# Kernel optimization log

Measured on AMD Instinct MI355X. Metric: run time of the kernel, lower is better.

The kernel has to match this reference:

```python
import jax, jax.numpy as jnp
import numpy as np

B, C, W, H = 256, 1, 512, 512
D0, D1 = 64, 64            # input_dims: crop/resample target
LATENT = 1024
HIST = 8                   # transformer_history_size (also attention heads)
DEPTH = 4
HEADS = 8
DIM_HEAD = 64              # n_heads arg is used as dim_head
INNER = HEADS * DIM_HEAD   # 512
MLP = LATENT
NCLS = 1000
EPS = 1e-5
RESNET_GAIN = 2.0 ** 7     # 7 identity ResidualBlocks, each does x += x


def setup_inputs() -> dict:
    key = jax.random.key(0)
    ks = jax.random.split(key, 12)
    def rn(k, shape):
        return jax.random.normal(k, shape, jnp.float32) * 0.02
    return dict(
        x=jax.random.normal(ks[0], (B, C, W, H), jnp.float32),
        transformation=jax.random.uniform(ks[1], (B, 4), dtype=jnp.float32),
        history=jnp.zeros((HIST, B, LATENT), jnp.float32),
        w_img=rn(ks[2], (D0 * D1, LATENT)), b_img=jnp.zeros((LATENT,), jnp.float32),
        ln1_s=jnp.ones((DEPTH, LATENT), jnp.float32), ln1_b=jnp.zeros((DEPTH, LATENT), jnp.float32),
        w_qkv=rn(ks[3], (DEPTH, LATENT, 3 * INNER)),
        w_o=rn(ks[4], (DEPTH, INNER, LATENT)), b_o=jnp.zeros((DEPTH, LATENT), jnp.float32),
        ln2_s=jnp.ones((DEPTH, LATENT), jnp.float32), ln2_b=jnp.zeros((DEPTH, LATENT), jnp.float32),
        w_ff1=rn(ks[5], (DEPTH, LATENT, MLP)), b_ff1=jnp.zeros((DEPTH, MLP), jnp.float32),
        w_ff2=rn(ks[6], (DEPTH, MLP, LATENT)), b_ff2=jnp.zeros((DEPTH, LATENT), jnp.float32),
        w_cls=rn(ks[7], (HIST * LATENT, NCLS)), b_cls=jnp.zeros((NCLS,), jnp.float32),
        w_tr=rn(ks[8], (HIST * LATENT, 4)), b_tr=jnp.zeros((4,), jnp.float32),
    )


def _ln(x, s, b):
    m = x.mean(-1, keepdims=True)
    v = x.var(-1, keepdims=True)
    return (x - m) / jnp.sqrt(v + EPS) * s + b


def _crop_one(img, sc):
    # img [C,W,H], sc = [px, py, zx, zy]; nearest crop+resample to (D0, D1)
    px, py, zx, zy = sc[0], sc[1], sc[2], sc[3]
    x1 = px * (W - D0)
    y1 = py * (H - D1)
    xs = jnp.minimum(W - x1, zx * (W - D0) + D0)
    ys = jnp.minimum(H - y1, zy * (H - D1) + D1)
    xi = jnp.clip((jnp.floor(jnp.arange(D0, dtype=jnp.float32) / D0 * xs) + x1).astype(jnp.int32), 0, W - 1)
    yi = jnp.clip((jnp.floor(jnp.arange(D1, dtype=jnp.float32) / D1 * ys) + y1).astype(jnp.int32), 0, H - 1)
    # itertools.product(c, xi, yi) ordering == reshape(-1) of [C, D0, D1]
    return img[:, xi[:, None], yi[None, :]].reshape(-1)


def _forward(x, transformation, history, w_img, b_img, ln1_s, ln1_b, w_qkv, w_o, b_o,
             ln2_s, ln2_b, w_ff1, b_ff1, w_ff2, b_ff2, w_cls, b_cls, w_tr, b_tr):
    crops = jax.vmap(_crop_one)(x, transformation)          # [B, C*D0*D1]
    feats = crops * RESNET_GAIN                             # ResNet18 == scale by 2^7
    image_latent = feats @ w_img + b_img                    # [B, LATENT]
    # history.append(latent); take last HIST; stack dim=1 -> [B, HIST, LATENT]
    hist = jnp.transpose(history, (1, 0, 2))                # [B, HIST, LATENT]
    z = jnp.concatenate([hist[:, 1:], image_latent[:, None, :]], axis=1)
    scale = DIM_HEAD ** -0.5
    for i in range(DEPTH):
        h = _ln(z, ln1_s[i], ln1_b[i])
        qkv = h @ w_qkv[i]                                  # [B, HIST, 3*INNER]
        q, k, v = jnp.split(qkv, 3, axis=-1)
        q = q.reshape(B, HIST, HEADS, DIM_HEAD).transpose(0, 2, 1, 3)
        k = k.reshape(B, HIST, HEADS, DIM_HEAD).transpose(0, 2, 1, 3)
        v = v.reshape(B, HIST, HEADS, DIM_HEAD).transpose(0, 2, 1, 3)
        attn = jax.nn.softmax(jnp.einsum('bhid,bhjd->bhij', q, k) * scale, axis=-1)
        o = jnp.einsum('bhij,bhjd->bhid', attn, v).transpose(0, 2, 1, 3).reshape(B, HIST, INNER)
        z = o @ w_o[i] + b_o[i] + z
        h2 = _ln(z, ln2_s[i], ln2_b[i])
        z = jax.nn.gelu(h2 @ w_ff1[i] + b_ff1[i], approximate=False) @ w_ff2[i] + b_ff2[i] + z
    tl = z.reshape(B, HIST * LATENT)
    class_pred = tl @ w_cls + b_cls                         # [B, NCLS]
    transform_pred = jax.nn.sigmoid(tl @ w_tr + b_tr)       # [B, 4]
    return class_pred, transform_pred


def reference(x, transformation, history, w_img, b_img, ln1_s, ln1_b, w_qkv, w_o, b_o,
              ln2_s, ln2_b, w_ff1, b_ff1, w_ff2, b_ff2, w_cls, b_cls, w_tr, b_tr):
    return _forward(x, transformation, history, w_img, b_img, ln1_s, ln1_b, w_qkv, w_o, b_o,
                    ln2_s, ln2_b, w_ff1, b_ff1, w_ff2, b_ff2, w_cls, b_cls, w_tr, b_tr)
```

## Files before the change

kernel.cpp:

```cpp
#include <hip/hip_runtime.h>
#include <cstdint>
#include <cstddef>

typedef __attribute__((ext_vector_type(8))) __bf16 bf16x8;
typedef __attribute__((ext_vector_type(8))) unsigned short u16x8;
typedef __attribute__((ext_vector_type(4))) float f32x4;
typedef __attribute__((ext_vector_type(4))) unsigned short u16x4;

__device__ __forceinline__ unsigned short f2bf(float f) {
  unsigned int u = __builtin_bit_cast(unsigned int, f);
  u += 0x7fffu + ((u >> 16) & 1u);
  return (unsigned short)(u >> 16);
}
__device__ __forceinline__ float bf2f(unsigned short u) {
  return __builtin_bit_cast(float, ((unsigned int)u) << 16);
}

__device__ void wcast_tile(char* smemc, int bid,
    const float* s_img, const float* s_qkv, const float* s_o,
    const float* s_ff1, const float* s_ff2, const float* s_cls,
    unsigned short* d_img, unsigned short* d_qkv, unsigned short* d_o,
    unsigned short* d_ff1, unsigned short* d_ff2, unsigned short* d_cls) {
  float (*tile)[65] = (float (*)[65])smemc;
  const float* src; unsigned short* dst; int K, N, Npad, rel;
  if (bid < 1024)       { src = s_img; dst = d_img; K = 4096; N = 1024; Npad = 1024; rel = bid; }
  else if (bid < 2560)  { rel = bid - 1024; int l = rel / 384; rel -= l * 384;
                          src = s_qkv + (size_t)l * 1024 * 1536; dst = d_qkv + (size_t)l * 1536 * 1024;
                          K = 1024; N = 1536; Npad = 1536; }
  else if (bid < 3072)  { rel = bid - 2560; int l = rel / 128; rel -= l * 128;
                          src = s_o   + (size_t)l * 512 * 1024;  dst = d_o   + (size_t)l * 1024 * 512;
                          K = 512;  N = 1024; Npad = 1024; }
  else if (bid < 4096)  { rel = bid - 3072; int l = rel / 256; rel -= l * 256;
                          src = s_ff1 + (size_t)l * 1024 * 1024; dst = d_ff1 + (size_t)l * 1024 * 1024;
                          K = 1024; N = 1024; Npad = 1024; }
  else if (bid < 5120)  { rel = bid - 4096; int l = rel / 256; rel -= l * 256;
                          src = s_ff2 + (size_t)l * 1024 * 1024; dst = d_ff2 + (size_t)l * 1024 * 1024;
                          K = 1024; N = 1024; Npad = 1024; }
  else                  { rel = bid - 5120; src = s_cls; dst = d_cls; K = 8192; N = 1000; Npad = 1024; }
  int tilesX = Npad >> 6;
  int nx = rel % tilesX, ky = rel / tilesX;
  int n0 = nx << 6, k0 = ky << 6;
  int t = threadIdx.x;
#pragma unroll
  for (int i = 0; i < 4; ++i) {
    int slot = t + i * 256;
    int kk = slot >> 4, cq = slot & 15;
    int n = n0 + cq * 4;
    float4 v;
    if (n + 3 < N) v = *(const float4*)(src + (size_t)(k0 + kk) * N + n);
    else {
      v.x = v.y = v.z = v.w = 0.0f;
      if (n < N)     v.x = src[(size_t)(k0 + kk) * N + n];
      if (n + 1 < N) v.y = src[(size_t)(k0 + kk) * N + n + 1];
      if (n + 2 < N) v.z = src[(size_t)(k0 + kk) * N + n + 2];
      if (n + 3 < N) v.w = src[(size_t)(k0 + kk) * N + n + 3];
    }
    tile[kk][cq * 4 + 0] = v.x;
    tile[kk][cq * 4 + 1] = v.y;
    tile[kk][cq * 4 + 2] = v.z;
    tile[kk][cq * 4 + 3] = v.w;
  }
  __syncthreads();
#pragma unroll
  for (int i = 0; i < 4; ++i) {
    int slot = t + i * 256;
    int n = slot >> 4, kq = slot & 15;
    u16x4 o;
    o.x = f2bf(tile[kq * 4 + 0][n]);
    o.y = f2bf(tile[kq * 4 + 1][n]);
    o.z = f2bf(tile[kq * 4 + 2][n]);
    o.w = f2bf(tile[kq * 4 + 3][n]);
    *(u16x4*)(dst + (size_t)(n0 + n) * K + k0 + kq * 4) = o;
  }
}

template <int BK, int ITERS>
__device__ __forceinline__ void stage_tile(const unsigned short* __restrict__ g, int ld,
                                           int k0, char* lbase, int tid) {
  constexpr int CH = BK / 8;
#pragma unroll
  for (int it = 0; it < ITERS; ++it) {
    int c = tid + it * 256;
    int r = c / CH;
    int slot = c & (CH - 1);
    int gc = slot ^ (r & (CH - 1));
    const unsigned short* src = g + (size_t)r * ld + (k0 + gc * 8);
    char* dst = lbase + c * 16;
    __builtin_amdgcn_global_load_lds((__attribute__((address_space(1))) void*)src,
                                     (__attribute__((address_space(3))) void*)dst, 16, 0, 0);
  }
}

template <int BK>
__device__ __forceinline__ bf16x8 ld_frag(const char* base, int row, int k8) {
  constexpr int CH = BK / 8;
  int off = row * (BK * 2) + ((k8 ^ (row & (CH - 1))) << 4);
  return *(const bf16x8*)(base + off);
}

template <int TN, int ACT, int OMODE, bool RES, int BK>
__device__ void gemm_tile(char* smem,
    const unsigned short* __restrict__ A, int lda,
    const unsigned short* __restrict__ BT, int ldb, int Kloop,
    const float* __restrict__ bias, const float* __restrict__ res,
    float* __restrict__ outF, unsigned short* __restrict__ outB,
    int ldC, int Nstore, int m0, int n0, int koff) {
  constexpr int MR = (TN == 64) ? 2 : 4;
  constexpr int ABYTES = 128 * BK * 2;
  constexpr int BUFS = (128 + TN) * BK * 2;
  constexpr int AITERS = BK / 16;
  constexpr int BITERS = TN * BK / 2048;
  const int tid = threadIdx.x;
  const int lane = tid & 63;
  const int wid = tid >> 6;
  const int rowbase = (TN == 64) ? wid * 32 : (wid >> 1) * 64;
  const int colbase = (TN == 64) ? 0 : (wid & 1) * 64;
  const unsigned short* Ag = A + (size_t)m0 * lda + koff;
  const unsigned short* Bg = BT + (size_t)n0 * ldb + koff;
  f32x4 acc[MR][4];
#pragma unroll
  for (int m = 0; m < MR; m++)
#pragma unroll
    for (int n = 0; n < 4; n++) acc[m][n] = 0.f;
  const int nt = Kloop / BK;
  stage_tile<BK, AITERS>(Ag, lda, 0, smem, tid);
  stage_tile<BK, BITERS>(Bg, ldb, 0, smem + ABYTES, tid);
  __syncthreads();
  int cur = 0;
  const int rA = lane & 15, kq = lane >> 4;
  for (int t = 0; t < nt; ++t) {
    if (t + 1 < nt) {
      stage_tile<BK, AITERS>(Ag, lda, (t + 1) * BK, smem + (cur ^ 1) * BUFS, tid);
      stage_tile<BK, BITERS>(Bg, ldb, (t + 1) * BK, smem + (cur ^ 1) * BUFS + ABYTES, tid);
    }
    const char* la = smem + cur * BUFS;
    const char* lb = la + ABYTES;
#pragma unroll
    for (int kk = 0; kk < BK / 32; ++kk) {
      int k8 = kk * 4 + kq;
      bf16x8 af[MR], bfr[4];
#pragma unroll
      for (int m = 0; m < MR; m++) af[m] = ld_frag<BK>(la, rowbase + m * 16 + rA, k8);
#pragma unroll
      for (int n = 0; n < 4; n++) bfr[n] = ld_frag<BK>(lb, colbase + n * 16 + rA, k8);
#pragma unroll
      for (int m = 0; m < MR; m++)
#pragma unroll
        for (int n = 0; n < 4; n++)
          acc[m][n] = __builtin_amdgcn_mfma_f32_16x16x32_bf16(af[m], bfr[n], acc[m][n], 0, 0, 0);
    }
    __syncthreads();
    cur ^= 1;
  }
  const int rb = m0 + rowbase + (kq << 2);
  const int cb = n0 + colbase + rA;
#pragma unroll
  for (int m = 0; m < MR; m++)
#pragma unroll
    for (int n = 0; n < 4; n++) {
      int cg = cb + n * 16;
      if (cg >= Nstore) continue;
      float bv = bias ? bias[cg] : 0.0f;
#pragma unroll
      for (int j = 0; j < 4; j++) {
        int rg = rb + m * 16 + j;
        float v = acc[m][n][j] + bv;
        if (RES) v += res[(size_t)rg * ldC + cg];
        if (ACT == 1) v = 0.5f * v * (1.0f + erff(v * 0.70710678118654752f));
        if (OMODE == 0) {
          outF[(size_t)rg * ldC + cg] = v;
        } else if (OMODE == 1) {
          outB[(size_t)rg * ldC + cg] = f2bf(v);
        } else {
          outF[(size_t)rg * ldC + cg] = v;
          outB[(size_t)rg * ldC + cg] = f2bf(v);
        }
      }
    }
}

#define SLABW 200
__global__ __launch_bounds__(256) void qkvattn(
    const unsigned short* __restrict__ h,
    const unsigned short* __restrict__ BTq,
    unsigned short* __restrict__ obuf) {
  __shared__ __align__(16) char smem[65536];
  const int tid = threadIdx.x, lane = tid & 63, wid = tid >> 6;
  const int p = blockIdx.x;
  const int xslot = p & 7, rem = p >> 3;
  const int hh = rem & 7;
  const int my = xslot + 8 * (rem >> 3);
  const int m0 = my << 6;
  const int wr = wid >> 1, wc = wid & 1;
  const unsigned short* Ag = h + (size_t)m0 * 1024;
  const unsigned short* Bseg0 = BTq + (size_t)(hh * 64) * 1024;
  const unsigned short* Bseg1 = BTq + (size_t)(512 + hh * 64) * 1024;
  const unsigned short* Bseg2 = BTq + (size_t)(1024 + hh * 64) * 1024;
  constexpr int BUFS = 32768;
  f32x4 acc[2][6];
#pragma unroll
  for (int m = 0; m < 2; m++)
#pragma unroll
    for (int n = 0; n < 6; n++) acc[m][n] = 0.f;
  const int rA = lane & 15, kq = lane >> 4;
  stage_tile<64, 2>(Ag, 1024, 0, smem, tid);
  stage_tile<64, 2>(Bseg0, 1024, 0, smem + 8192, tid);
  stage_tile<64, 2>(Bseg1, 1024, 0, smem + 16384, tid);
  stage_tile<64, 2>(Bseg2, 1024, 0, smem + 24576, tid);
  __syncthreads();
  int cur = 0;
  for (int t = 0; t < 16; ++t) {
    if (t + 1 < 16) {
      char* nb = smem + (cur ^ 1) * BUFS;
      stage_tile<64, 2>(Ag, 1024, (t + 1) << 6, nb, tid);
      stage_tile<64, 2>(Bseg0, 1024, (t + 1) << 6, nb + 8192, tid);
      stage_tile<64, 2>(Bseg1, 1024, (t + 1) << 6, nb + 16384, tid);
      stage_tile<64, 2>(Bseg2, 1024, (t + 1) << 6, nb + 24576, tid);
    }
    const char* la = smem + cur * BUFS;
#pragma unroll
    for (int kk = 0; kk < 2; ++kk) {
      int k8 = kk * 4 + kq;
      bf16x8 af[2], bfr[6];
#pragma unroll
      for (int m = 0; m < 2; m++) af[m] = ld_frag<64>(la, wr * 32 + m * 16 + rA, k8);
#pragma unroll
      for (int n = 0; n < 6; n++) {
        int cidx = wc * 96 + n * 16 + rA;
        bfr[n] = ld_frag<64>(la + 8192 + (cidx >> 6) * 8192, cidx & 63, k8);
      }
#pragma unroll
      for (int m = 0; m < 2; m++)
#pragma unroll
        for (int n = 0; n < 6; n++)
          acc[m][n] = __builtin_amdgcn_mfma_f32_16x16x32_bf16(af[m], bfr[n], acc[m][n], 0, 0, 0);
    }
    __syncthreads();
    cur ^= 1;
  }
  unsigned short* slab = (unsigned short*)smem;
  float* Sb = (float*)(smem + 64 * SLABW * 2 + wid * 512);
#pragma unroll
  for (int m = 0; m < 2; m++)
#pragma unroll
    for (int n = 0; n < 6; n++) {
      int r = wr * 32 + m * 16 + (kq << 2);
      int c = wc * 96 + n * 16 + rA;
#pragma unroll
      for (int j = 0; j < 4; j++) slab[(size_t)(r + j) * SLABW + c] = f2bf(acc[m][n][j]);
    }
  __syncthreads();
  {
#pragma unroll
    for (int e = 0; e < 2; ++e) {
      int idx = e * 64 + lane;
      int bl = idx >> 6;
      int i = (idx >> 3) & 7, j = idx & 7;
      int rb8 = wid * 16 + bl * 8;
      const u16x8* qrow = (const u16x8*)(slab + (size_t)(rb8 + i) * SLABW);
      const u16x8* krow = (const u16x8*)(slab + (size_t)(rb8 + j) * SLABW + 64);
      float s = 0.f;
#pragma unroll
      for (int q8 = 0; q8 < 8; ++q8) {
        u16x8 qv = qrow[q8], kv = krow[q8];
#pragma unroll
        for (int u = 0; u < 8; ++u) s = fmaf(bf2f(qv[u]), bf2f(kv[u]), s);
      }
      Sb[bl * 64 + i * 8 + j] = s * 0.125f;
    }
    if (lane < 16) {
      float4 r0 = ((const float4*)(Sb + lane * 8))[0];
      float4 r1 = ((const float4*)(Sb + lane * 8))[1];
      float mx = fmaxf(fmaxf(fmaxf(r0.x, r0.y), fmaxf(r0.z, r0.w)),
                       fmaxf(fmaxf(r1.x, r1.y), fmaxf(r1.z, r1.w)));
      float e0 = expf(r0.x - mx), e1 = expf(r0.y - mx), e2 = expf(r0.z - mx), e3 = expf(r0.w - mx);
      float e4_ = expf(r1.x - mx), e5 = expf(r1.y - mx), e6 = expf(r1.z - mx), e7 = expf(r1.w - mx);
      float inv = 1.0f / (e0 + e1 + e2 + e3 + e4_ + e5 + e6 + e7);
      ((float4*)(Sb + lane * 8))[0] = make_float4(e0 * inv, e1 * inv, e2 * inv, e3 * inv);
      ((float4*)(Sb + lane * 8))[1] = make_float4(e4_ * inv, e5 * inv, e6 * inv, e7 * inv);
    }
#pragma unroll
    for (int bl = 0; bl < 2; ++bl) {
      int rb8 = wid * 16 + bl * 8;
      float vreg[8];
#pragma unroll
      for (int jj = 0; jj < 8; ++jj) vreg[jj] = bf2f(slab[(size_t)(rb8 + jj) * SLABW + 128 + lane]);
      int browg = (my * 8 + wid * 2 + bl) * 8;
#pragma unroll
      for (int i = 0; i < 8; ++i) {
        float4 p0 = ((const float4*)(Sb + (bl * 64 + i * 8)))[0];
        float4 p1 = ((const float4*)(Sb + (bl * 64 + i * 8)))[1];
        float o = p0.x * vreg[0] + p0.y * vreg[1] + p0.z * vreg[2] + p0.w * vreg[3] +
                  p1.x * vreg[4] + p1.y * vreg[5] + p1.z * vreg[6] + p1.w * vreg[7];
        obuf[(size_t)(browg + i) * 512 + hh * 64 + lane] = f2bf(o);
      }
    }
  }
}

__global__ __launch_bounds__(256) void front1(
    const float* __restrict__ x, const float* __restrict__ tr, const float* __restrict__ hist,
    const float* __restrict__ w_img, const float* __restrict__ w_qkv, const float* __restrict__ w_o,
    const float* __restrict__ w_ff1, const float* __restrict__ w_ff2, const float* __restrict__ w_cls,
    unsigned short* BT_img, unsigned short* BT_qkv, unsigned short* BT_o,
    unsigned short* BT_ff1, unsigned short* BT_ff2, unsigned short* BT_cls,
    unsigned short* feats, float* z) {
  __shared__ __align__(16) char smem[16640];
  int bid = blockIdx.x;
  int tid = threadIdx.x;
  if (bid < 1024) {
    wcast_tile(smem, bid, w_img, w_qkv, w_o, w_ff1, w_ff2, w_cls,
               BT_img, BT_qkv, BT_o, BT_ff1, BT_ff2, BT_cls);
  } else if (bid < 1280) {
    int b = bid - 1024;
    int* xi = (int*)smem;
    int* yi = xi + 64;
    float px = tr[b * 4 + 0], py = tr[b * 4 + 1], zx = tr[b * 4 + 2], zy = tr[b * 4 + 3];
    float x1 = __fmul_rn(px, 448.0f);
    float y1 = __fmul_rn(py, 448.0f);
    float xs = fminf(__fsub_rn(512.0f, x1), __fadd_rn(__fmul_rn(zx, 448.0f), 64.0f));
    float ys = fminf(__fsub_rn(512.0f, y1), __fadd_rn(__fmul_rn(zy, 448.0f), 64.0f));
    if (tid < 64) {
      float u = __fmul_rn(__fmul_rn((float)tid, 0.015625f), xs);
      int v = (int)(__fadd_rn(floorf(u), x1));
      xi[tid] = min(max(v, 0), 511);
    } else if (tid < 128) {
      int tt = tid - 64;
      float u = __fmul_rn(__fmul_rn((float)tt, 0.015625f), ys);
      int v = (int)(__fadd_rn(floorf(u), y1));
      yi[tt] = min(max(v, 0), 511);
    }
    __syncthreads();
    const float* img = x + (size_t)b * 262144;
    for (int p = tid; p < 4096; p += 256) {
      int i = p >> 6, j = p & 63;
      float val = img[xi[i] * 512 + yi[j]] * 128.0f;
      feats[(size_t)b * 4096 + p] = f2bf(val);
    }
  } else {
    int idx = (bid - 1280) * 256 + tid;
    int off = idx * 4;
    int b = off / 7168;
    int r = off - b * 7168;
    int i = r >> 10, c = r & 1023;
    float4 v = *(const float4*)(hist + (size_t)(i + 1) * 262144 + (size_t)b * 1024 + c);
    *(float4*)(z + (size_t)b * 8192 + i * 1024 + c) = v;
  }
}

__global__ __launch_bounds__(256) void k_img(
    const unsigned short* __restrict__ feats, const unsigned short* __restrict__ BT_img,
    float* __restrict__ part,
    const float* __restrict__ w_img, const float* __restrict__ w_qkv, const float* __restrict__ w_o,
    const float* __restrict__ w_ff1, const float* __restrict__ w_ff2, const float* __restrict__ w_cls,
    unsigned short* BT_img_d, unsigned short* BT_qkv, unsigned short* BT_o,
    unsigned short* BT_ff1, unsigned short* BT_ff2, unsigned short* BT_cls) {
  __shared__ __align__(16) char smem[49152];
  int bid = blockIdx.x;
  if (bid < 256) {
    int xslot = bid & 7, rem = bid >> 3;
    int nx = rem & 15, chi = rem >> 4;
    int c = xslot + 8 * chi;
    int sk = c >> 1, my = c & 1;
    gemm_tile<64, 0, 0, false, 64>(smem, feats, 4096, BT_img, 4096, 512,
                                   nullptr, nullptr, part + (size_t)sk * 262144, nullptr,
                                   1024, 1024, my * 128, nx * 64, sk * 512);
  } else {
    wcast_tile(smem, 1024 + bid - 256, w_img, w_qkv, w_o, w_ff1, w_ff2, w_cls,
               BT_img_d, BT_qkv, BT_o, BT_ff1, BT_ff2, BT_cls);
  }
}

__device__ __forceinline__ void ln_row(const float* __restrict__ z, int row,
                                       const float* __restrict__ sc, const float* __restrict__ bi,
                                       unsigned short* __restrict__ h) {
  int lane = threadIdx.x & 63;
  const float* zr = z + (size_t)row * 1024;
  float4 v[4];
  float s = 0.f, q = 0.f;
#pragma unroll
  for (int i = 0; i < 4; i++) {
    v[i] = *(const float4*)(zr + lane * 4 + i * 256);
    s += v[i].x + v[i].y + v[i].z + v[i].w;
    q += v[i].x * v[i].x + v[i].y * v[i].y + v[i].z * v[i].z + v[i].w * v[i].w;
  }
#pragma unroll
  for (int off = 32; off; off >>= 1) { s += __shfl_xor(s, off); q += __shfl_xor(q, off); }
  float mean = s * (1.0f / 1024.0f);
  float var = q * (1.0f / 1024.0f) - mean * mean;
  float rstd = rsqrtf(var + 1e-5f);
  u16x4* out = (u16x4*)(h + (size_t)row * 1024);
#pragma unroll
  for (int i = 0; i < 4; i++) {
    int c = lane * 4 + i * 256;
    float4 sv = *(const float4*)(sc + c);
    float4 bv = *(const float4*)(bi + c);
    u16x4 o;
    o.x = f2bf((v[i].x - mean) * rstd * sv.x + bv.x);
    o.y = f2bf((v[i].y - mean) * rstd * sv.y + bv.y);
    o.z = f2bf((v[i].z - mean) * rstd * sv.z + bv.z);
    o.w = f2bf((v[i].w - mean) * rstd * sv.w + bv.w);
    out[lane + i * 64] = o;
  }
}

__global__ __launch_bounds__(256) void imgred_ln(
    const float* __restrict__ part, const float* __restrict__ b_img, float* __restrict__ z,
    const float* __restrict__ sc, const float* __restrict__ bi,
    unsigned short* __restrict__ h) {
  __shared__ float ws[8];
  int m = blockIdx.x, tid = threadIdx.x;
  int lane = tid & 63, wid = tid >> 6;
  int c = tid * 4;
  float4 a = {0.f, 0.f, 0.f, 0.f};
  for (int p = 0; p < 8; ++p) {
    float4 v = *(const float4*)(part + (size_t)p * 262144 + m * 1024 + c);
    a.x += v.x; a.y += v.y; a.z += v.z; a.w += v.w;
  }
  float4 bv = *(const float4*)(b_img + c);
  a.x += bv.x; a.y += bv.y; a.z += bv.z; a.w += bv.w;
  *(float4*)(z + (size_t)m * 8192 + 7168 + c) = a;
  float s = a.x + a.y + a.z + a.w;
  float q = a.x * a.x + a.y * a.y + a.z * a.z + a.w * a.w;
#pragma unroll
  for (int off = 32; off; off >>= 1) { s += __shfl_xor(s, off); q += __shfl_xor(q, off); }
  if (lane == 0) { ws[wid * 2] = s; ws[wid * 2 + 1] = q; }
  __syncthreads();
  float S4 = ws[0] + ws[2] + ws[4] + ws[6];
  float Q4 = ws[1] + ws[3] + ws[5] + ws[7];
  float mean = S4 * (1.0f / 1024.0f);
  float var = Q4 * (1.0f / 1024.0f) - mean * mean;
  float rstd = rsqrtf(var + 1e-5f);
  float4 sv = *(const float4*)(sc + c);
  float4 bb = *(const float4*)(bi + c);
  u16x4 o;
  o.x = f2bf((a.x - mean) * rstd * sv.x + bb.x);
  o.y = f2bf((a.y - mean) * rstd * sv.y + bb.y);
  o.z = f2bf((a.z - mean) * rstd * sv.z + bb.z);
  o.w = f2bf((a.w - mean) * rstd * sv.w + bb.w);
  *(u16x4*)(h + (size_t)(m * 8 + 7) * 1024 + c) = o;
#pragma unroll
  for (int rr = 0; rr < 2; ++rr) {
    int r = wid * 2 + rr;
    if (r < 7) ln_row(z, m * 8 + r, sc, bi, h);
  }
}

__global__ __launch_bounds__(256) void ln_kernel(const float* __restrict__ z,
                                                 const float* __restrict__ sc,
                                                 const float* __restrict__ bi,
                                                 unsigned short* __restrict__ h) {
  int row = blockIdx.x * 4 + (threadIdx.x >> 6);
  ln_row(z, row, sc, bi, h);
}

template <int TN, int ACT, int OMODE, bool RES, int BK>
__global__ __launch_bounds__(256) void gemm_k(
    const unsigned short* __restrict__ A, int lda,
    const unsigned short* __restrict__ BT, int ldb, int Kloop,
    const float* __restrict__ bias, const float* __restrict__ res,
    float* __restrict__ outF, unsigned short* __restrict__ outB,
    int ldC, int Nstore) {
  constexpr int BUFS = (128 + TN) * BK * 2;
  __shared__ __align__(16) char smem[2 * BUFS];
  int p = blockIdx.x;
  int xslot = p & 7, rem = p >> 3;
  int nx = rem & 15;
  int my = xslot + 8 * (rem >> 4);
  gemm_tile<TN, ACT, OMODE, RES, BK>(smem, A, lda, BT, ldb, Kloop, bias, res, outF, outB,
                                     ldC, Nstore, my * 128, nx * TN, 0);
}

__global__ __launch_bounds__(256) void k_cls(
    const unsigned short* __restrict__ tl, const unsigned short* __restrict__ BT_cls,
    float* __restrict__ part,
    const float* __restrict__ z, const float* __restrict__ w_tr,
    const float* __restrict__ b_tr, float* __restrict__ outF) {
  __shared__ __align__(16) char smem[49152];
  int bid = blockIdx.x;
  int tid = threadIdx.x;
  if (bid < 256) {
    int xslot = bid & 7, rem = bid >> 3;
    int nx = rem & 15, chi = rem >> 4;
    int c = xslot + 8 * chi;
    int sk = c >> 1, my = c & 1;
    gemm_tile<64, 0, 0, false, 64>(smem, tl, 8192, BT_cls, 8192, 1024,
                                   nullptr, nullptr, part + (size_t)sk * 262144, nullptr,
                                   1024, 1024, my * 128, nx * 64, sk * 1024);
  } else {
    int m = bid - 256;
    const float* row = z + (size_t)m * 8192;
    float a0 = 0.f, a1 = 0.f, a2 = 0.f, a3 = 0.f;
    for (int k = tid; k < 8192; k += 256) {
      float xv = row[k];
      const float* wr = w_tr + (size_t)k * 4;
      a0 += xv * wr[0]; a1 += xv * wr[1]; a2 += xv * wr[2]; a3 += xv * wr[3];
    }
    float (*red)[4] = (float (*)[4])smem;
    red[tid][0] = a0; red[tid][1] = a1; red[tid][2] = a2; red[tid][3] = a3;
    __syncthreads();
    for (int s = 128; s > 0; s >>= 1) {
      if (tid < s) {
#pragma unroll
        for (int o = 0; o < 4; o++) red[tid][o] += red[tid + s][o];
      }
      __syncthreads();
    }
    if (tid < 4) {
      float v = red[0][tid] + b_tr[tid];
      outF[256000 + m * 4 + tid] = 1.0f / (1.0f + expf(-v));
    }
  }
}

__global__ __launch_bounds__(256) void clsred(const float* __restrict__ part,
                                              const float* __restrict__ b_cls,
                                              float* __restrict__ outF) {
  int m = blockIdx.x, c = threadIdx.x * 4;
  float4 a = {0.f, 0.f, 0.f, 0.f};
  for (int p = 0; p < 8; ++p) {
    float4 v = *(const float4*)(part + (size_t)p * 262144 + m * 1024 + c);
    a.x += v.x; a.y += v.y; a.z += v.z; a.w += v.w;
  }
  if (c >= 1000) return;
  float* drow = outF + (size_t)m * 1000;
  float vals[4] = {a.x, a.y, a.z, a.w};
  if (c + 3 < 1000) {
    *(float4*)(drow + c) = make_float4(vals[0] + b_cls[c], vals[1] + b_cls[c + 1],
                                       vals[2] + b_cls[c + 2], vals[3] + b_cls[c + 3]);
  } else {
    for (int j = 0; j < 4 && c + j < 1000; ++j) drow[c + j] = vals[j] + b_cls[c + j];
  }
}

extern "C" void kernel_launch(void* const* d_in, const int* in_sizes, int n_in,
                              void* d_out, int out_size, void* d_ws, size_t ws_size,
                              hipStream_t stream) {
  const float* x      = (const float*)d_in[0];
  const float* tr     = (const float*)d_in[1];
  const float* hist   = (const float*)d_in[2];
  const float* w_img  = (const float*)d_in[3];
  const float* b_img  = (const float*)d_in[4];
  const float* ln1_s  = (const float*)d_in[5];
  const float* ln1_b  = (const float*)d_in[6];
  const float* w_qkv  = (const float*)d_in[7];
  const float* w_o    = (const float*)d_in[8];
  const float* b_o    = (const float*)d_in[9];
  const float* ln2_s  = (const float*)d_in[10];
  const float* ln2_b  = (const float*)d_in[11];
  const float* w_ff1  = (const float*)d_in[12];
  const float* b_ff1  = (const float*)d_in[13];
  const float* w_ff2  = (const float*)d_in[14];
  const float* b_ff2  = (const float*)d_in[15];
  const float* w_cls  = (const float*)d_in[16];
  const float* b_cls  = (const float*)d_in[17];
  const float* w_tr   = (const float*)d_in[18];
  const float* b_tr   = (const float*)d_in[19];
  float* outF = (float*)d_out;

  char* w = (char*)d_ws;
  auto alloc = [&](size_t bytes) { char* p = w; w += (bytes + 255) & ~(size_t)255; return p; };
  unsigned short* BT_img = (unsigned short*)alloc((size_t)1024 * 4096 * 2);
  unsigned short* BT_qkv = (unsigned short*)alloc((size_t)4 * 1536 * 1024 * 2);
  unsigned short* BT_o   = (unsigned short*)alloc((size_t)4 * 1024 * 512 * 2);
  unsigned short* BT_ff1 = (unsigned short*)alloc((size_t)4 * 1024 * 1024 * 2);
  unsigned short* BT_ff2 = (unsigned short*)alloc((size_t)4 * 1024 * 1024 * 2);
  unsigned short* BT_cls = (unsigned short*)alloc((size_t)1024 * 8192 * 2);
  unsigned short* feats  = (unsigned short*)alloc((size_t)256 * 4096 * 2);
  float*          z      = (float*)alloc((size_t)2048 * 1024 * 4);
  unsigned short* h      = (unsigned short*)alloc((size_t)2048 * 1024 * 2);
  unsigned short* obuf   = (unsigned short*)alloc((size_t)2048 * 512 * 2);
  unsigned short* g      = (unsigned short*)alloc((size_t)2048 * 1024 * 2);
  float*          part   = (float*)alloc((size_t)8 * 256 * 1024 * 4);
  if ((size_t)(w - (char*)d_ws) > ws_size) return;

  front1<<<3072, 256, 0, stream>>>(x, tr, hist, w_img, w_qkv, w_o, w_ff1, w_ff2, w_cls,
                                   BT_img, BT_qkv, BT_o, BT_ff1, BT_ff2, BT_cls, feats, z);
  k_img<<<6400, 256, 0, stream>>>(feats, BT_img, part,
                                  w_img, w_qkv, w_o, w_ff1, w_ff2, w_cls,
                                  BT_img, BT_qkv, BT_o, BT_ff1, BT_ff2, BT_cls);
  imgred_ln<<<256, 256, 0, stream>>>(part, b_img, z, ln1_s, ln1_b, h);

  for (int i = 0; i < 4; ++i) {
    const unsigned short* Wq = BT_qkv + (size_t)i * 1536 * 1024;
    const unsigned short* Wo = BT_o   + (size_t)i * 1024 * 512;
    const unsigned short* W1 = BT_ff1 + (size_t)i * 1024 * 1024;
    const unsigned short* W2 = BT_ff2 + (size_t)i * 1024 * 1024;
    if (i > 0)
      ln_kernel<<<512, 256, 0, stream>>>(z, ln1_s + i * 1024, ln1_b + i * 1024, h);
    qkvattn<<<256, 256, 0, stream>>>(h, Wq, obuf);
    gemm_k<64, 0, 0, true, 64><<<256, 256, 0, stream>>>(
        obuf, 512, Wo, 512, 512, b_o + i * 1024, z, z, nullptr, 1024, 1024);
    ln_kernel<<<512, 256, 0, stream>>>(z, ln2_s + i * 1024, ln2_b + i * 1024, h);
    gemm_k<64, 1, 1, false, 64><<<256, 256, 0, stream>>>(
        h, 1024, W1, 1024, 1024, b_ff1 + i * 1024, nullptr, nullptr, g, 1024, 1024);
    if (i < 3) {
      gemm_k<64, 0, 0, true, 64><<<256, 256, 0, stream>>>(
          g, 1024, W2, 1024, 1024, b_ff2 + i * 1024, z, z, nullptr, 1024, 1024);
    } else {
      gemm_k<64, 0, 2, true, 64><<<256, 256, 0, stream>>>(
          g, 1024, W2, 1024, 1024, b_ff2 + i * 1024, z, z, h, 1024, 1024);
    }
  }

  k_cls<<<512, 256, 0, stream>>>(h, BT_cls, part, z, w_tr, b_tr, outF);
  clsred<<<256, 256, 0, stream>>>(part, b_cls, outF);
}
```

Before: 336.8 us.

## Store residual stream z in bf16 and move history copy into k_img

```diff
diff --git a/kernel.cpp b/kernel.cpp
--- a/kernel.cpp
+++ b/kernel.cpp
@@ -102,7 +102,7 @@
 __device__ void gemm_tile(char* smem,
     const unsigned short* __restrict__ A, int lda,
     const unsigned short* __restrict__ BT, int ldb, int Kloop,
-    const float* __restrict__ bias, const float* __restrict__ res,
+    const float* __restrict__ bias, const unsigned short* __restrict__ res,
     float* __restrict__ outF, unsigned short* __restrict__ outB,
     int ldC, int Nstore, int m0, int n0, int koff) {
   constexpr int MR = (TN == 64) ? 2 : 4;
@@ -165,14 +165,11 @@
       for (int j = 0; j < 4; j++) {
         int rg = rb + m * 16 + j;
         float v = acc[m][n][j] + bv;
-        if (RES) v += res[(size_t)rg * ldC + cg];
+        if (RES) v += bf2f(res[(size_t)rg * ldC + cg]);
         if (ACT == 1) v = 0.5f * v * (1.0f + erff(v * 0.70710678118654752f));
         if (OMODE == 0) {
           outF[(size_t)rg * ldC + cg] = v;
-        } else if (OMODE == 1) {
-          outB[(size_t)rg * ldC + cg] = f2bf(v);
         } else {
-          outF[(size_t)rg * ldC + cg] = v;
           outB[(size_t)rg * ldC + cg] = f2bf(v);
         }
       }
@@ -299,19 +296,19 @@
 }
 
 __global__ __launch_bounds__(256) void front1(
-    const float* __restrict__ x, const float* __restrict__ tr, const float* __restrict__ hist,
+    const float* __restrict__ x, const float* __restrict__ tr,
     const float* __restrict__ w_img, const float* __restrict__ w_qkv, const float* __restrict__ w_o,
     const float* __restrict__ w_ff1, const float* __restrict__ w_ff2, const float* __restrict__ w_cls,
     unsigned short* BT_img, unsigned short* BT_qkv, unsigned short* BT_o,
     unsigned short* BT_ff1, unsigned short* BT_ff2, unsigned short* BT_cls,
-    unsigned short* feats, float* z) {
+    unsigned short* feats) {
   __shared__ __align__(16) char smem[16640];
   int bid = blockIdx.x;
   int tid = threadIdx.x;
   if (bid < 1024) {
     wcast_tile(smem, bid, w_img, w_qkv, w_o, w_ff1, w_ff2, w_cls,
                BT_img, BT_qkv, BT_o, BT_ff1, BT_ff2, BT_cls);
-  } else if (bid < 1280) {
+  } else {
     int b = bid - 1024;
     int* xi = (int*)smem;
     int* yi = xi + 64;
@@ -337,20 +334,12 @@
       float val = img[xi[i] * 512 + yi[j]] * 128.0f;
       feats[(size_t)b * 4096 + p] = f2bf(val);
     }
-  } else {
-    int idx = (bid - 1280) * 256 + tid;
-    int off = idx * 4;
-    int b = off / 7168;
-    int r = off - b * 7168;
-    int i = r >> 10, c = r & 1023;
-    float4 v = *(const float4*)(hist + (size_t)(i + 1) * 262144 + (size_t)b * 1024 + c);
-    *(float4*)(z + (size_t)b * 8192 + i * 1024 + c) = v;
   }
 }
 
 __global__ __launch_bounds__(256) void k_img(
     const unsigned short* __restrict__ feats, const unsigned short* __restrict__ BT_img,
-    float* __restrict__ part,
+    float* __restrict__ part, const float* __restrict__ hist, unsigned short* __restrict__ z,
     const float* __restrict__ w_img, const float* __restrict__ w_qkv, const float* __restrict__ w_o,
     const float* __restrict__ w_ff1, const float* __restrict__ w_ff2, const float* __restrict__ w_cls,
     unsigned short* BT_img_d, unsigned short* BT_qkv, unsigned short* BT_o,
@@ -365,47 +354,67 @@
     gemm_tile<64, 0, 0, false, 64>(smem, feats, 4096, BT_img, 4096, 512,
                                    nullptr, nullptr, part + (size_t)sk * 262144, nullptr,
                                    1024, 1024, my * 128, nx * 64, sk * 512);
-  } else {
+  } else if (bid < 6400) {
     wcast_tile(smem, 1024 + bid - 256, w_img, w_qkv, w_o, w_ff1, w_ff2, w_cls,
                BT_img_d, BT_qkv, BT_o, BT_ff1, BT_ff2, BT_cls);
-  }
-}
-
-__device__ __forceinline__ void ln_row(const float* __restrict__ z, int row,
+  } else {
+    int idx = (bid - 6400) * 256 + threadIdx.x;
+    int off = idx * 4;
+    int b = off / 7168;
+    int r = off - b * 7168;
+    int i = r >> 10, c = r & 1023;
+    float4 v = *(const float4*)(hist + (size_t)(i + 1) * 262144 + (size_t)b * 1024 + c);
+    u16x4 o;
+    o.x = f2bf(v.x); o.y = f2bf(v.y); o.z = f2bf(v.z); o.w = f2bf(v.w);
+    *(u16x4*)(z + (size_t)b * 8192 + i * 1024 + c) = o;
+  }
+}
+
+__device__ __forceinline__ void ln_row(const unsigned short* __restrict__ z, int row,
                                        const float* __restrict__ sc, const float* __restrict__ bi,
                                        unsigned short* __restrict__ h) {
   int lane = threadIdx.x & 63;
-  const float* zr = z + (size_t)row * 1024;
-  float4 v[4];
+  const unsigned short* zr = z + (size_t)row * 1024;
+  float vf[16];
   float s = 0.f, q = 0.f;
 #pragma unroll
-  for (int i = 0; i < 4; i++) {
-    v[i] = *(const float4*)(zr + lane * 4 + i * 256);
-    s += v[i].x + v[i].y + v[i].z + v[i].w;
-    q += v[i].x * v[i].x + v[i].y * v[i].y + v[i].z * v[i].z + v[i].w * v[i].w;
+  for (int i = 0; i < 2; i++) {
+    u16x8 v = *(const u16x8*)(zr + lane * 8 + i * 512);
+#pragma unroll
+    for (int u = 0; u < 8; u++) {
+      float f = bf2f(v[u]);
+      vf[i * 8 + u] = f;
+      s += f; q += f * f;
+    }
   }
 #pragma unroll
   for (int off = 32; off; off >>= 1) { s += __shfl_xor(s, off); q += __shfl_xor(q, off); }
   float mean = s * (1.0f / 1024.0f);
   float var = q * (1.0f / 1024.0f) - mean * mean;
   float rstd = rsqrtf(var + 1e-5f);
-  u16x4* out = (u16x4*)(h + (size_t)row * 1024);
-#pragma unroll
-  for (int i = 0; i < 4; i++) {
-    int c = lane * 4 + i * 256;
-    float4 sv = *(const float4*)(sc + c);
-    float4 bv = *(const float4*)(bi + c);
-    u16x4 o;
-    o.x = f2bf((v[i].x - mean) * rstd * sv.x + bv.x);
-    o.y = f2bf((v[i].y - mean) * rstd * sv.y + bv.y);
-    o.z = f2bf((v[i].z - mean) * rstd * sv.z + bv.z);
-    o.w = f2bf((v[i].w - mean) * rstd * sv.w + bv.w);
-    out[lane + i * 64] = o;
+#pragma unroll
+  for (int i = 0; i < 2; i++) {
+    int c = lane * 8 + i * 512;
+    float4 s0 = *(const float4*)(sc + c);
+    float4 s1 = *(const float4*)(sc + c + 4);
+    float4 b0 = *(const float4*)(bi + c);
+    float4 b1 = *(const float4*)(bi + c + 4);
+    u16x8 o;
+    o[0] = f2bf((vf[i * 8 + 0] - mean) * rstd * s0.x + b0.x);
+    o[1] = f2bf((vf[i * 8 + 1] - mean) * rstd * s0.y + b0.y);
+    o[2] = f2bf((vf[i * 8 + 2] - mean) * rstd * s0.z + b0.z);
+    o[3] = f2bf((vf[i * 8 + 3] - mean) * rstd * s0.w + b0.w);
+    o[4] = f2bf((vf[i * 8 + 4] - mean) * rstd * s1.x + b1.x);
+    o[5] = f2bf((vf[i * 8 + 5] - mean) * rstd * s1.y + b1.y);
+    o[6] = f2bf((vf[i * 8 + 6] - mean) * rstd * s1.z + b1.z);
+    o[7] = f2bf((vf[i * 8 + 7] - mean) * rstd * s1.w + b1.w);
+    *(u16x8*)(h + (size_t)row * 1024 + c) = o;
   }
 }
 
 __global__ __launch_bounds__(256) void imgred_ln(
-    const float* __restrict__ part, const float* __restrict__ b_img, float* __restrict__ z,
+    const float* __restrict__ part, const float* __restrict__ b_img,
+    unsigned short* __restrict__ z,
     const float* __restrict__ sc, const float* __restrict__ bi,
     unsigned short* __restrict__ h) {
   __shared__ float ws[8];
@@ -419,7 +428,9 @@
   }
   float4 bv = *(const float4*)(b_img + c);
   a.x += bv.x; a.y += bv.y; a.z += bv.z; a.w += bv.w;
-  *(float4*)(z + (size_t)m * 8192 + 7168 + c) = a;
+  u16x4 zo;
+  zo.x = f2bf(a.x); zo.y = f2bf(a.y); zo.z = f2bf(a.z); zo.w = f2bf(a.w);
+  *(u16x4*)(z + (size_t)m * 8192 + 7168 + c) = zo;
   float s = a.x + a.y + a.z + a.w;
   float q = a.x * a.x + a.y * a.y + a.z * a.z + a.w * a.w;
 #pragma unroll
@@ -446,7 +457,7 @@
   }
 }
 
-__global__ __launch_bounds__(256) void ln_kernel(const float* __restrict__ z,
+__global__ __launch_bounds__(256) void ln_kernel(const unsigned short* __restrict__ z,
                                                  const float* __restrict__ sc,
                                                  const float* __restrict__ bi,
                                                  unsigned short* __restrict__ h) {
@@ -458,7 +469,7 @@
 __global__ __launch_bounds__(256) void gemm_k(
     const unsigned short* __restrict__ A, int lda,
     const unsigned short* __restrict__ BT, int ldb, int Kloop,
-    const float* __restrict__ bias, const float* __restrict__ res,
+    const float* __restrict__ bias, const unsigned short* __restrict__ res,
     float* __restrict__ outF, unsigned short* __restrict__ outB,
     int ldC, int Nstore) {
   constexpr int BUFS = (128 + TN) * BK * 2;
@@ -472,9 +483,8 @@
 }
 
 __global__ __launch_bounds__(256) void k_cls(
-    const unsigned short* __restrict__ tl, const unsigned short* __restrict__ BT_cls,
-    float* __restrict__ part,
-    const float* __restrict__ z, const float* __restrict__ w_tr,
+    const unsigned short* __restrict__ z, const unsigned short* __restrict__ BT_cls,
+    float* __restrict__ part, const float* __restrict__ w_tr,
     const float* __restrict__ b_tr, float* __restrict__ outF) {
   __shared__ __align__(16) char smem[49152];
   int bid = blockIdx.x;
@@ -484,15 +494,15 @@
     int nx = rem & 15, chi = rem >> 4;
     int c = xslot + 8 * chi;
     int sk = c >> 1, my = c & 1;
-    gemm_tile<64, 0, 0, false, 64>(smem, tl, 8192, BT_cls, 8192, 1024,
+    gemm_tile<64, 0, 0, false, 64>(smem, z, 8192, BT_cls, 8192, 1024,
                                    nullptr, nullptr, part + (size_t)sk * 262144, nullptr,
                                    1024, 1024, my * 128, nx * 64, sk * 1024);
   } else {
     int m = bid - 256;
-    const float* row = z + (size_t)m * 8192;
+    const unsigned short* row = z + (size_t)m * 8192;
     float a0 = 0.f, a1 = 0.f, a2 = 0.f, a3 = 0.f;
     for (int k = tid; k < 8192; k += 256) {
-      float xv = row[k];
+      float xv = bf2f(row[k]);
       const float* wr = w_tr + (size_t)k * 4;
       a0 += xv * wr[0]; a1 += xv * wr[1]; a2 += xv * wr[2]; a3 += xv * wr[3];
     }
@@ -567,16 +577,16 @@
   unsigned short* BT_ff2 = (unsigned short*)alloc((size_t)4 * 1024 * 1024 * 2);
   unsigned short* BT_cls = (unsigned short*)alloc((size_t)1024 * 8192 * 2);
   unsigned short* feats  = (unsigned short*)alloc((size_t)256 * 4096 * 2);
-  float*          z      = (float*)alloc((size_t)2048 * 1024 * 4);
+  unsigned short* z      = (unsigned short*)alloc((size_t)2048 * 1024 * 2);
   unsigned short* h      = (unsigned short*)alloc((size_t)2048 * 1024 * 2);
   unsigned short* obuf   = (unsigned short*)alloc((size_t)2048 * 512 * 2);
   unsigned short* g      = (unsigned short*)alloc((size_t)2048 * 1024 * 2);
   float*          part   = (float*)alloc((size_t)8 * 256 * 1024 * 4);
   if ((size_t)(w - (char*)d_ws) > ws_size) return;
 
-  front1<<<3072, 256, 0, stream>>>(x, tr, hist, w_img, w_qkv, w_o, w_ff1, w_ff2, w_cls,
-                                   BT_img, BT_qkv, BT_o, BT_ff1, BT_ff2, BT_cls, feats, z);
-  k_img<<<6400, 256, 0, stream>>>(feats, BT_img, part,
+  front1<<<1280, 256, 0, stream>>>(x, tr, w_img, w_qkv, w_o, w_ff1, w_ff2, w_cls,
+                                   BT_img, BT_qkv, BT_o, BT_ff1, BT_ff2, BT_cls, feats);
+  k_img<<<8192, 256, 0, stream>>>(feats, BT_img, part, hist, z,
                                   w_img, w_qkv, w_o, w_ff1, w_ff2, w_cls,
                                   BT_img, BT_qkv, BT_o, BT_ff1, BT_ff2, BT_cls);
   imgred_ln<<<256, 256, 0, stream>>>(part, b_img, z, ln1_s, ln1_b, h);
@@ -589,20 +599,15 @@
     if (i > 0)
       ln_kernel<<<512, 256, 0, stream>>>(z, ln1_s + i * 1024, ln1_b + i * 1024, h);
     qkvattn<<<256, 256, 0, stream>>>(h, Wq, obuf);
-    gemm_k<64, 0, 0, true, 64><<<256, 256, 0, stream>>>(
-        obuf, 512, Wo, 512, 512, b_o + i * 1024, z, z, nullptr, 1024, 1024);
+    gemm_k<64, 0, 1, true, 64><<<256, 256, 0, stream>>>(
+        obuf, 512, Wo, 512, 512, b_o + i * 1024, z, nullptr, z, 1024, 1024);
     ln_kernel<<<512, 256, 0, stream>>>(z, ln2_s + i * 1024, ln2_b + i * 1024, h);
     gemm_k<64, 1, 1, false, 64><<<256, 256, 0, stream>>>(
         h, 1024, W1, 1024, 1024, b_ff1 + i * 1024, nullptr, nullptr, g, 1024, 1024);
-    if (i < 3) {
-      gemm_k<64, 0, 0, true, 64><<<256, 256, 0, stream>>>(
-          g, 1024, W2, 1024, 1024, b_ff2 + i * 1024, z, z, nullptr, 1024, 1024);
-    } else {
-      gemm_k<64, 0, 2, true, 64><<<256, 256, 0, stream>>>(
-          g, 1024, W2, 1024, 1024, b_ff2 + i * 1024, z, z, h, 1024, 1024);
-    }
-  }
-
-  k_cls<<<512, 256, 0, stream>>>(h, BT_cls, part, z, w_tr, b_tr, outF);
+    gemm_k<64, 0, 1, true, 64><<<256, 256, 0, stream>>>(
+        g, 1024, W2, 1024, 1024, b_ff2 + i * 1024, z, nullptr, z, 1024, 1024);
+  }
+
+  k_cls<<<512, 256, 0, stream>>>(z, BT_cls, part, w_tr, b_tr, outF);
   clsred<<<256, 256, 0, stream>>>(part, b_cls, outF);
 }
```

Measured after the change: 323.1 us. 4.1% less time.
